# Kernel tuning notes

Measured on AMD Instinct MI355X. Metric: run time of the kernel, lower is better.

The kernel has to match this reference:

```python
import jax, jax.numpy as jnp
import numpy as np

B, T, IN = 8, 1000, 80
CONV = 256
CCEP = 222            # ltv_out_channels
FFT_SIZE = 1024
HOP = 256
WIN = 2 * HOP         # 512
PAD = (FFT_SIZE - CCEP) // 2   # 401
NFFT = 2048


def _conv1d_same(x, W, b, groups):
    # x: (B,T,C); W: (O, C//groups, 3); equivalent to torch Conv1d pad=2 then [1:-1]
    y = jax.lax.conv_general_dilated(
        jnp.transpose(x, (0, 2, 1)), W, (1,), [(1, 1)],
        feature_group_count=groups,
        dimension_numbers=('NCH', 'OIH', 'NCH'))
    return jnp.transpose(y, (0, 2, 1)) + b


def _forward(x, z, W1, b1, W2, b2, W3, b3, W4, b4):
    Bx, Tx, _ = x.shape
    # ---- ConvLayers ----
    h = jax.nn.relu(_conv1d_same(x, W1, b1, 1))
    h = jax.nn.relu(_conv1d_same(h, W2, b2, 8))
    h = jax.nn.relu(_conv1d_same(h, W3, b3, 8))
    ccep = _conv1d_same(h, W4, b4, 1)            # (B,T,222)
    q = jnp.arange(1, CCEP // 2 + 1, dtype=x.dtype)
    quef = jnp.concatenate([q[::-1], q])          # [111..1,1..111]
    ccep = ccep / quef
    # ---- ccep -> impulse (log-magnitude cepstrum -> minimum-ish phase impulse) ----
    c = jnp.pad(ccep, ((0, 0), (0, 0), (PAD, PAD)))           # (B,T,1024)
    Y = jnp.fft.fft(c, n=FFT_SIZE, axis=-1)
    mag = jnp.power(10.0, Y.real)
    imp = jnp.fft.ifft(mag * jnp.exp(1j * Y.imag), n=FFT_SIZE, axis=-1).real  # (B,T,1024)
    # ---- time-varying impulse convolution (cross-correlation per frame) ----
    L = z.shape[-1]
    zz = z.reshape(Bx, 1, L)
    zp = jnp.pad(zz, ((0, 0), (0, 0), (WIN // 2 - 1, WIN // 2)))
    starts = jnp.arange(Tx) * HOP
    frames = zp[:, :, starts[:, None] + jnp.arange(WIN)]       # (B,1,T,512)
    fp = jnp.pad(frames, ((0, 0), (0, 0), (0, 0), (FFT_SIZE // 2 - 1, FFT_SIZE // 2)))  # len 1535
    # corr[s] = sum_k fp[s+k] * imp[k], s in [0,512); linear corr via zero-padded FFT
    Fz = jnp.fft.rfft(fp, n=NFFT, axis=-1)                     # (B,1,T,NFFT//2+1)
    Fy = jnp.fft.rfft(imp, n=NFFT, axis=-1)[:, None]           # (B,1,T,NFFT//2+1)
    corr = jnp.fft.irfft(Fz * jnp.conj(Fy), n=NFFT, axis=-1)[..., :WIN]  # (B,1,T,512)
    # ---- overlap-add ----
    n = jnp.arange(WIN, dtype=x.dtype)
    win = 0.5 * (1.0 - jnp.cos(2.0 * jnp.pi * n / WIN))        # periodic hann, win_norm=1
    zw = corr * win
    l, r = zw[..., :HOP], zw[..., HOP:]
    out = l + jnp.roll(r, 1, axis=2)
    return out.reshape(Bx, 1, Tx * HOP)


def setup_inputs() -> dict:
    key = jax.random.key(0)
    ks = jax.random.split(key, 12)
    x = jax.random.normal(ks[0], (B, T, IN), dtype=jnp.float32)
    z = jax.random.normal(ks[1], (B, 1, T * HOP), dtype=jnp.float32)
    def w(k, o, i, kk, scale):
        return jax.random.normal(k, (o, i, kk), dtype=jnp.float32) * (scale / np.sqrt(i * kk))
    W1 = w(ks[2], CONV, IN, 3, 1.0)
    b1 = jnp.zeros((CONV,), jnp.float32)
    W2 = w(ks[3], CONV, CONV // 8, 3, 1.0)
    b2 = jnp.zeros((CONV,), jnp.float32)
    W3 = w(ks[4], CONV, CONV // 8, 3, 1.0)
    b3 = jnp.zeros((CONV,), jnp.float32)
    W4 = w(ks[5], CCEP, CONV, 3, 0.01)   # small scale keeps 10**(.) well-conditioned
    b4 = jnp.zeros((CCEP,), jnp.float32)
    return {"x": x, "z": z, "W1": W1, "b1": b1, "W2": W2, "b2": b2,
            "W3": W3, "b3": b3, "W4": W4, "b4": b4}


def reference(x, z, W1, b1, W2, b2, W3, b3, W4, b4):
    return _forward(x, z, W1, b1, W2, b2, W3, b3, W4, b4)
```

## Files before the change

### kernel.cpp

```cpp
#include <hip/hip_runtime.h>
#include <hip/hip_bf16.h>

#define T_LEN 1000
#define B_N 8
#define IN_CH 80
#define CONV_CH 256
#define CCEP_N 222

typedef short s8v __attribute__((ext_vector_type(8)));
typedef float f16v __attribute__((ext_vector_type(16)));

#define TWO_PI 6.28318530717958647692f

__global__ __launch_bounds__(256) void k_prep(
    const float* __restrict__ W1, const float* __restrict__ W2,
    const float* __restrict__ W3, const float* __restrict__ W4,
    float* __restrict__ Wt1, float* __restrict__ Wt2, float* __restrict__ Wt3,
    __hip_bfloat16* __restrict__ Wc, float2* __restrict__ twTab,
    float* __restrict__ winTab) {
  const int bid = blockIdx.x, tid = threadIdx.x;
  if (bid < 240) {
    int e = bid * 256 + tid;
    int p = e & 3;
    int r = e >> 2;
    int o = r & 255;
    int s = r >> 8;
    int k = s % 3, i4 = s / 3;
    Wt1[e] = W1[o * 240 + (4 * i4 + p) * 3 + k];
  } else if (bid < 336) {
    int e = (bid - 240) * 256 + tid;
    int p = e & 3;
    int r = e >> 2;
    int o = r & 255;
    int s = r >> 8;
    int k = s % 3, i4 = s / 3;
    Wt2[e] = W2[o * 96 + (4 * i4 + p) * 3 + k];
  } else if (bid < 432) {
    int e = (bid - 336) * 256 + tid;
    int p = e & 3;
    int r = e >> 2;
    int o = r & 255;
    int s = r >> 8;
    int k = s % 3, i4 = s / 3;
    Wt3[e] = W3[o * 96 + (4 * i4 + p) * 3 + k];
  } else if (bid < 1200) {
    int e = (bid - 432) * 256 + tid;
    int kloc = e & 31, n = (e >> 5) & 255, chg = e >> 13;
    int kp = chg * 32 + kloc;
    int kappa = kp >> 8, i = kp & 255;
    float v = 0.f;
    if (n < CCEP_N) {
      float invq = 1.f / (float)((n < 111) ? (111 - n) : (n - 110));
      v = W4[n * 768 + i * 3 + kappa] * invq;
    }
    Wc[e] = __float2bfloat16(v);
  } else {
    int e = (bid - 1200) * 256 + tid;
    if (e < 1020) {
      int Q, off;
      if (e < 768)       { Q = 256; off = 0; }
      else if (e < 960)  { Q = 64;  off = 768; }
      else if (e < 1008) { Q = 16;  off = 960; }
      else               { Q = 4;   off = 1008; }
      int rem = e - off;
      int r = rem / Q, pos = rem - r * Q;
      float ang = (TWO_PI * (float)((r + 1) * pos)) / (float)(4 * Q);
      float s, c;
      sincosf(ang, &s, &c);
      twTab[e] = make_float2(c, s);
    } else if (e < 1532) {
      int n = e - 1020;
      winTab[n] = (0.5f - 0.5f * cosf(TWO_PI * (float)n / 512.f)) * (1.f / 1024.f);
    }
  }
}

template <int NJ, int NI4, int PITCH, int NA2>
__device__ __forceinline__ void conv_acc(const float* __restrict__ abase,
    const float4* __restrict__ wq, float* __restrict__ acc) {
  float4 c0 = wq[0], c1 = wq[256], c2 = wq[512];
  for (int ig = 0; ig < NI4; ++ig) {
    const int nx = (ig + 1 < NI4) ? (ig + 1) : (NI4 - 1);
    float4 n0 = wq[(nx * 3 + 0) * 256];
    float4 n1 = wq[(nx * 3 + 1) * 256];
    float4 n2 = wq[(nx * 3 + 2) * 256];
#pragma unroll
    for (int s = 0; s < 4; ++s) {
      const float* row = abase + (4 * ig + s) * PITCH;
      float a[2 * NA2];
#pragma unroll
      for (int u = 0; u < NA2; ++u)
        *(float2*)&a[2 * u] = *(const float2*)(row + 2 * u);
      const float f0 = ((const float*)&c0)[s];
      const float f1 = ((const float*)&c1)[s];
      const float f2 = ((const float*)&c2)[s];
#pragma unroll
      for (int jl = 0; jl < NJ; ++jl) {
        acc[jl] = fmaf(a[jl], f0, acc[jl]);
        acc[jl] = fmaf(a[jl + 1], f1, acc[jl]);
        acc[jl] = fmaf(a[jl + 2], f2, acc[jl]);
      }
    }
    c0 = n0; c1 = n1; c2 = n2;
  }
}

__global__ __launch_bounds__(256) void k_convall(const float* __restrict__ x,
    const float* __restrict__ Wt1, const float* __restrict__ b1,
    const float* __restrict__ Wt2, const float* __restrict__ b2,
    const float* __restrict__ Wt3, const float* __restrict__ b3,
    __hip_bfloat16* __restrict__ out) {
  const int b = blockIdx.y;
  const int t0 = blockIdx.x * 10;
  const int o = threadIdx.x;
  const int cb = (o >> 5) << 5;
  __shared__ float xs[IN_CH * 18];
  __shared__ float hs1[CONV_CH * 14];
  __shared__ float hs2[CONV_CH * 14];
  for (int e = threadIdx.x; e < 16 * IN_CH; e += 256) {
    int r = e / IN_CH, c = e - r * IN_CH;
    int t = t0 - 3 + r;
    xs[c * 18 + r] = (t >= 0 && t < T_LEN) ? x[(b * T_LEN + t) * IN_CH + c] : 0.f;
  }
  __syncthreads();
  {
    float acc[14];
    const float bv = b1[o];
#pragma unroll
    for (int j = 0; j < 14; j++) acc[j] = bv;
    conv_acc<14, 20, 18, 8>(&xs[0], (const float4*)Wt1 + o, acc);
#pragma unroll
    for (int j = 0; j < 14; j++) {
      int t = t0 - 2 + j;
      hs1[o * 14 + j] = (t >= 0 && t < T_LEN) ? fmaxf(acc[j], 0.f) : 0.f;
    }
  }
  __syncthreads();
  {
    float acc[12];
    const float bv = b2[o];
#pragma unroll
    for (int j = 0; j < 12; j++) acc[j] = bv;
    conv_acc<12, 8, 14, 7>(&hs1[cb * 14], (const float4*)Wt2 + o, acc);
#pragma unroll
    for (int j = 0; j < 12; j++) {
      int t = t0 - 1 + j;
      hs2[o * 14 + j] = (t >= 0 && t < T_LEN) ? fmaxf(acc[j], 0.f) : 0.f;
    }
  }
  __syncthreads();
  {
    float acc[10];
    const float bv = b3[o];
#pragma unroll
    for (int j = 0; j < 10; j++) acc[j] = bv;
    conv_acc<10, 8, 14, 6>(&hs2[cb * 14], (const float4*)Wt3 + o, acc);
#pragma unroll
    for (int j = 0; j < 10; j++)
      out[(b * T_LEN + t0 + j) * CONV_CH + o] = __float2bfloat16(fmaxf(acc[j], 0.f));
  }
}

#define APITCH 264
#define BPITCH 40
#define PSTRIDE 1792000
__global__ __launch_bounds__(256) void k_conv4m(
    const __hip_bfloat16* __restrict__ h3, const __hip_bfloat16* __restrict__ Wc,
    const float* __restrict__ bias, float* __restrict__ Pbase) {
  const int mb = blockIdx.x, b = blockIdx.y, ks = blockIdx.z;
  float* __restrict__ P = Pbase + (size_t)ks * PSTRIDE;
  const int t0 = mb * 64;
  const int tid = threadIdx.x;
  const int w = tid >> 6, lane = tid & 63;
  const int wm = w >> 1, wn = w & 1;
  const int lm = lane & 31, half = lane >> 5;

  __shared__ short h3s[67 * APITCH];
  __shared__ short Bs[2][256 * BPITCH];

  const ushort* h3u = (const ushort*)h3;
  for (int g = tid; g < 67 * 64; g += 256) {
    int rr = g >> 6, c4 = g & 63;
    int t = t0 + rr - 1;
    uint2 v = make_uint2(0u, 0u);
    if (t >= 0 && t < T_LEN)
      v = *(const uint2*)(h3u + (b * T_LEN + t) * CONV_CH + c4 * 4);
    *(uint2*)(h3s + rr * APITCH + c4 * 4) = v;
  }

  const ushort* Wu = (const ushort*)(Wc) + (size_t)(ks * 6) * 8192;
#pragma unroll
  for (int it = 0; it < 4; ++it) {
    int idx = (it * 256 + tid) * 8;
    uint4 v = *(const uint4*)(Wu + idx);
    int n = idx >> 5, kloc = idx & 31;
    *(uint4*)(Bs[0] + n * BPITCH + kloc) = v;
  }
  __syncthreads();

  f16v acc0 = {}, acc1 = {}, acc2 = {}, acc3 = {};

  for (int ch = 0; ch < 6; ++ch) {
    const int p = ch & 1;
    if (ch < 5) {
      const ushort* src = Wu + (ch + 1) * 8192;
#pragma unroll
      for (int it = 0; it < 4; ++it) {
        int idx = (it * 256 + tid) * 8;
        uint4 v = *(const uint4*)(src + idx);
        int n = idx >> 5, kloc = idx & 31;
        *(uint4*)(Bs[p ^ 1] + n * BPITCH + kloc) = v;
      }
    }
#pragma unroll
    for (int s = 0; s < 2; ++s) {
      int k0 = ks * 192 + ch * 32 + s * 16;
      int kappa = k0 >> 8, i0 = k0 & 255;
      s8v a = *(const s8v*)(h3s + (wm * 32 + lm + kappa) * APITCH + i0 + half * 8);
      const short* bp = Bs[p] + (wn * 128 + lm) * BPITCH + s * 16 + half * 8;
      s8v b0 = *(const s8v*)(bp);
      s8v b1 = *(const s8v*)(bp + 32 * BPITCH);
      s8v b2 = *(const s8v*)(bp + 64 * BPITCH);
      s8v b3 = *(const s8v*)(bp + 96 * BPITCH);
      acc0 = __builtin_amdgcn_mfma_f32_32x32x16_bf16(a, b0, acc0, 0, 0, 0);
      acc1 = __builtin_amdgcn_mfma_f32_32x32x16_bf16(a, b1, acc1, 0, 0, 0);
      acc2 = __builtin_amdgcn_mfma_f32_32x32x16_bf16(a, b2, acc2, 0, 0, 0);
      acc3 = __builtin_amdgcn_mfma_f32_32x32x16_bf16(a, b3, acc3, 0, 0, 0);
    }
    __syncthreads();
  }

  const int col = lm;
#pragma unroll
  for (int nt = 0; nt < 4; ++nt) {
    int c = wn * 128 + nt * 32 + col;
    if (c >= CCEP_N) continue;
    float bq = 0.f;
    if (ks == 0) {
      float invq = 1.f / (float)((c < 111) ? (111 - c) : (c - 110));
      bq = bias[c] * invq;
    }
    const f16v* A = (nt == 0) ? &acc0 : (nt == 1) ? &acc1 : (nt == 2) ? &acc2 : &acc3;
#pragma unroll
    for (int reg = 0; reg < 16; ++reg) {
      int row = (reg & 3) + 8 * (reg >> 2) + 4 * half;
      int t = t0 + wm * 32 + row;
      if (t < T_LEN)
        P[(size_t)(b * T_LEN + t) * 224 + c] = (*A)[reg] + bq;
    }
  }
}

__device__ __forceinline__ float2 cmul(float2 a, float2 b) {
  return make_float2(fmaf(a.x, b.x, -(a.y * b.y)), fmaf(a.x, b.y, a.y * b.x));
}
__device__ __forceinline__ float2 cadd(float2 a, float2 b) { return make_float2(a.x + b.x, a.y + b.y); }
__device__ __forceinline__ float2 csub(float2 a, float2 b) { return make_float2(a.x - b.x, a.y - b.y); }

#define LIDX(i) ((i) + ((i) >> 2))

template <int Q, int OFF>
__device__ __forceinline__ void fwd_stage2(float2* __restrict__ A,
    float2* __restrict__ B, const float2* __restrict__ Tw, int j) {
  const int pos = j & (Q - 1);
  const int base = ((j - pos) << 2) + pos;
  float2 e1 = Tw[OFF + pos], e2 = Tw[OFF + Q + pos], e3 = Tw[OFF + 2 * Q + pos];
  const float2 w1 = make_float2(e1.x, -e1.y);
  const float2 w2 = make_float2(e2.x, -e2.y);
  const float2 w3 = make_float2(e3.x, -e3.y);
#pragma unroll
  for (int arr = 0; arr < 2; ++arr) {
    float2* X = arr ? B : A;
    float2 a = X[LIDX(base)], b = X[LIDX(base + Q)];
    float2 cc = X[LIDX(base + 2 * Q)], d = X[LIDX(base + 3 * Q)];
    float2 t0 = cadd(a, cc), t1 = csub(a, cc), t2 = cadd(b, d), bd = csub(b, d);
    float2 t3 = make_float2(bd.y, -bd.x);
    X[LIDX(base)]         = cadd(t0, t2);
    X[LIDX(base + Q)]     = cmul(cadd(t1, t3), w1);
    X[LIDX(base + 2 * Q)] = cmul(csub(t0, t2), w2);
    X[LIDX(base + 3 * Q)] = cmul(csub(t1, t3), w3);
  }
}

template <int Q, int OFF>
__device__ __forceinline__ void inv_stage_t(float2* __restrict__ X,
    const float2* __restrict__ Tw, int j) {
  const int pos = j & (Q - 1);
  const int base = ((j - pos) << 2) + pos;
  const float2 w1 = Tw[OFF + pos];
  const float2 w2 = Tw[OFF + Q + pos];
  const float2 w3 = Tw[OFF + 2 * Q + pos];
  float2 a = X[LIDX(base)];
  float2 b = cmul(X[LIDX(base + Q)], w1);
  float2 cc = cmul(X[LIDX(base + 2 * Q)], w2);
  float2 d = cmul(X[LIDX(base + 3 * Q)], w3);
  float2 t0 = cadd(a, cc), t1 = csub(a, cc), t2 = cadd(b, d), bd = csub(b, d);
  float2 t3 = make_float2(-bd.y, bd.x);
  X[LIDX(base)]         = cadd(t0, t2);
  X[LIDX(base + Q)]     = cadd(t1, t3);
  X[LIDX(base + 2 * Q)] = csub(t0, t2);
  X[LIDX(base + 3 * Q)] = csub(t1, t3);
}

__device__ __forceinline__ int rev4d(int v) {
  return ((v & 3) << 6) | (((v >> 2) & 3) << 4) | (((v >> 4) & 3) << 2) | ((v >> 6) & 3);
}

__global__ __launch_bounds__(256) void k_fft(const float* __restrict__ Pb,
    const float* __restrict__ z, const float2* __restrict__ twg,
    const float* __restrict__ wing, float* __restrict__ out,
    float* __restrict__ sbl, float* __restrict__ sbr) {
  const int u = blockIdx.x, b = blockIdx.y;
  const int tA = 2 * u, tB = tA + 1;
  const int btA = b * T_LEN + tA, btB = btA + 1;
  const int j = threadIdx.x;
  __shared__ float2 WlA[1280];
  __shared__ float2 WlB[1280];
  __shared__ float2 Tws[1020];
  for (int e = j; e < 1020; e += 256) Tws[e] = twg[e];

  const float* zb = z + b * 256000;
  float f0A = 0.f, fS, f1B = 0.f;
  {
    int zi0 = tA * 256 + j - 255;
    f0A = (zi0 >= 0) ? zb[zi0] : 0.f;
    fS = zb[tA * 256 + j + 1];
    int zi2 = tB * 256 + j + 1;
    f1B = (zi2 < 256000) ? zb[zi2] : 0.f;
  }
  float c1A = 0.f, c2A = 0.f, c1B = 0.f, c2B = 0.f;
  if (j >= 145) {
    int mA = btA * 224 + (j - 145), mB = btB * 224 + (j - 145);
    c1A = (Pb[mA] + Pb[mA + PSTRIDE]) + (Pb[mA + 2 * PSTRIDE] + Pb[mA + 3 * PSTRIDE]);
    c1B = (Pb[mB] + Pb[mB + PSTRIDE]) + (Pb[mB + 2 * PSTRIDE] + Pb[mB + 3 * PSTRIDE]);
  }
  if (j < 111) {
    int mA = btA * 224 + (j + 111), mB = btB * 224 + (j + 111);
    c2A = (Pb[mA] + Pb[mA + PSTRIDE]) + (Pb[mA + 2 * PSTRIDE] + Pb[mA + 3 * PSTRIDE]);
    c2B = (Pb[mB] + Pb[mB + PSTRIDE]) + (Pb[mB + 2 * PSTRIDE] + Pb[mB + 3 * PSTRIDE]);
  }
  __syncthreads();

  {
    float2 e1 = Tws[j], e2 = Tws[256 + j], e3 = Tws[512 + j];
    const float2 w1 = make_float2(e1.x, -e1.y);
    const float2 w2 = make_float2(e2.x, -e2.y);
    const float2 w3 = make_float2(e3.x, -e3.y);
    {
      float2 t0 = make_float2(c2A, f0A);
      float2 t1 = make_float2(-c2A, f0A);
      float2 t2 = make_float2(c1A, fS);
      float2 t3 = make_float2(fS, -c1A);
      WlA[LIDX(j)]       = cadd(t0, t2);
      WlA[LIDX(j + 256)] = cmul(cadd(t1, t3), w1);
      WlA[LIDX(j + 512)] = cmul(csub(t0, t2), w2);
      WlA[LIDX(j + 768)] = cmul(csub(t1, t3), w3);
    }
    {
      float2 t0 = make_float2(c2B, fS);
      float2 t1 = make_float2(-c2B, fS);
      float2 t2 = make_float2(c1B, f1B);
      float2 t3 = make_float2(f1B, -c1B);
      WlB[LIDX(j)]       = cadd(t0, t2);
      WlB[LIDX(j + 256)] = cmul(cadd(t1, t3), w1);
      WlB[LIDX(j + 512)] = cmul(csub(t0, t2), w2);
      WlB[LIDX(j + 768)] = cmul(csub(t1, t3), w3);
    }
  }
  __syncthreads();

  fwd_stage2<64, 768>(WlA, WlB, Tws, j);  __syncthreads();
  fwd_stage2<16, 960>(WlA, WlB, Tws, j);  __syncthreads();
  fwd_stage2<4, 1008>(WlA, WlB, Tws, j);  __syncthreads();

  const int base = 4 * j;
  float2 XA[4], XB[4];
  {
    float2 u0 = WlA[LIDX(base)], u1 = WlA[LIDX(base + 1)];
    float2 u2 = WlA[LIDX(base + 2)], u3 = WlA[LIDX(base + 3)];
    float2 t0 = cadd(u0, u2), t1 = csub(u0, u2), t2 = cadd(u1, u3), bd = csub(u1, u3);
    float2 t3 = make_float2(bd.y, -bd.x);
    XA[0] = cadd(t0, t2); XA[1] = cadd(t1, t3); XA[2] = csub(t0, t2); XA[3] = csub(t1, t3);
  }
  {
    float2 u0 = WlB[LIDX(base)], u1 = WlB[LIDX(base + 1)];
    float2 u2 = WlB[LIDX(base + 2)], u3 = WlB[LIDX(base + 3)];
    float2 t0 = cadd(u0, u2), t1 = csub(u0, u2), t2 = cadd(u1, u3), bd = csub(u1, u3);
    float2 t3 = make_float2(bd.y, -bd.x);
    XB[0] = cadd(t0, t2); XB[1] = cadd(t1, t3); XB[2] = csub(t0, t2); XB[3] = csub(t1, t3);
  }
#pragma unroll
  for (int q = 0; q < 4; ++q) { WlA[LIDX(base + q)] = XA[q]; WlB[LIDX(base + q)] = XB[q]; }
  __syncthreads();

  const int r0 = rev4d(j);
  const bool self0 = (r0 == 0);
  const int jp = self0 ? 0 : rev4d((256 - r0) & 255);
  float2 PA[4], PB[4];
#pragma unroll
  for (int q = 0; q < 4; ++q) { PA[q] = WlA[LIDX(4 * jp + q)]; PB[q] = WlB[LIDX(4 * jp + q)]; }
  float2 Z[4];
#pragma unroll
  for (int q = 0; q < 4; ++q) {
    float2 SA, SB;
    {
      float2 A = XA[q];
      float2 Bc = self0 ? PA[(4 - q) & 3] : PA[3 - q];
      float2 Y = make_float2(0.5f * (A.x + Bc.x), 0.5f * (A.y - Bc.y));
      float2 F = make_float2(0.5f * (A.y + Bc.y), -0.5f * (A.x - Bc.x));
      float mag = __expf(Y.x * 2.30258509299404568402f);
      float sy, cy;
      __sincosf(Y.y, &sy, &cy);
      float gr = mag * cy, gi = mag * sy;
      SA = make_float2(fmaf(F.x, gr, F.y * gi), fmaf(F.x, gi, -(F.y * gr)));
    }
    {
      float2 A = XB[q];
      float2 Bc = self0 ? PB[(4 - q) & 3] : PB[3 - q];
      float2 Y = make_float2(0.5f * (A.x + Bc.x), 0.5f * (A.y - Bc.y));
      float2 F = make_float2(0.5f * (A.y + Bc.y), -0.5f * (A.x - Bc.x));
      float mag = __expf(Y.x * 2.30258509299404568402f);
      float sy, cy;
      __sincosf(Y.y, &sy, &cy);
      float gr = mag * cy, gi = mag * sy;
      SB = make_float2(fmaf(F.x, gr, F.y * gi), fmaf(F.x, gi, -(F.y * gr)));
    }
    Z[q] = make_float2(SA.x - SB.y, SA.y + SB.x);
  }
  __syncthreads();

  {
    float2 t0 = cadd(Z[0], Z[2]), t1 = csub(Z[0], Z[2]), t2 = cadd(Z[1], Z[3]), bd = csub(Z[1], Z[3]);
    float2 t3 = make_float2(-bd.y, bd.x);
    WlA[LIDX(base)]     = cadd(t0, t2);
    WlA[LIDX(base + 1)] = cadd(t1, t3);
    WlA[LIDX(base + 2)] = csub(t0, t2);
    WlA[LIDX(base + 3)] = csub(t1, t3);
  }
  __syncthreads();

  inv_stage_t<4, 1008>(WlA, Tws, j);  __syncthreads();
  inv_stage_t<16, 960>(WlA, Tws, j);  __syncthreads();
  inv_stage_t<64, 768>(WlA, Tws, j);  __syncthreads();

  {
    float2 w1 = Tws[j], w2 = Tws[256 + j], w3 = Tws[512 + j];
    float2 a = WlA[LIDX(j)];
    float2 bb = cmul(WlA[LIDX(j + 256)], w1);
    float2 cc = cmul(WlA[LIDX(j + 512)], w2);
    float2 d = cmul(WlA[LIDX(j + 768)], w3);
    float2 t0 = cadd(a, cc), t1 = csub(a, cc), t2 = cadd(bb, d), bd = csub(bb, d);
    float2 t3 = make_float2(-bd.y, bd.x);
    float2 Cj    = cadd(t0, t2);
    float2 Cj256 = cadd(t1, t3);
    int n1 = 511 - j, n2 = 255 - j;
    float wn1 = wing[n1], wn2 = wing[n2];
    float vA_l = Cj256.x * wn2;
    float vAB  = Cj.x * wn1 + Cj256.y * wn2;
    float vB_r = Cj.y * wn1;
    out[(b * T_LEN + tB) * 256 + n2] = vAB;
    int su = (b * 500 + u) * 256 + n2;
    sbl[su] = vA_l;
    sbr[su] = vB_r;
  }
}

__global__ __launch_bounds__(256) void k_even(const float* __restrict__ sbl,
    const float* __restrict__ sbr, float* __restrict__ out) {
  int idx = blockIdx.x * 256 + threadIdx.x;
  int n = idx & 255;
  int bu = idx >> 8;
  int u = bu % 500, b = bu / 500;
  int up = (u == 0) ? 499 : u - 1;
  out[(b * T_LEN + 2 * u) * 256 + n] = sbl[idx] + sbr[(b * 500 + up) * 256 + n];
}

extern "C" void kernel_launch(void* const* d_in, const int* in_sizes, int n_in,
                              void* d_out, int out_size, void* d_ws, size_t ws_size,
                              hipStream_t stream) {
  const float* x  = (const float*)d_in[0];
  const float* z  = (const float*)d_in[1];
  const float* W1 = (const float*)d_in[2];
  const float* b1 = (const float*)d_in[3];
  const float* W2 = (const float*)d_in[4];
  const float* b2 = (const float*)d_in[5];
  const float* W3 = (const float*)d_in[6];
  const float* b3 = (const float*)d_in[7];
  const float* W4 = (const float*)d_in[8];
  const float* b4 = (const float*)d_in[9];

  float* ws   = (float*)d_ws;
  __hip_bfloat16* h3bf = (__hip_bfloat16*)ws;
  float* Pb   = ws + 1024000;
  float* sbl  = ws + 8192000;
  float* sbr  = ws + 9216000;
  float* Wt1  = ws + 10240000;
  float* Wt2  = ws + 10301440;
  float* Wt3  = ws + 10326016;
  __hip_bfloat16* Wc = (__hip_bfloat16*)(ws + 10350592);
  float2* twTab = (float2*)(ws + 10448896);
  float* winTab = ws + 10450944;
  float* out = (float*)d_out;

  dim3 blk(256);
  k_prep<<<1206, blk, 0, stream>>>(W1, W2, W3, W4, Wt1, Wt2, Wt3, Wc,
                                   twTab, winTab);

  dim3 cgrid10(T_LEN / 10, B_N);
  k_convall<<<cgrid10, blk, 0, stream>>>(x, Wt1, b1, Wt2, b2, Wt3, b3, h3bf);
  dim3 g4(16, B_N, 4);
  k_conv4m<<<g4, blk, 0, stream>>>(h3bf, Wc, b4, Pb);
  dim3 gf(T_LEN / 2, B_N);
  k_fft<<<gf, blk, 0, stream>>>(Pb, z, twTab, winTab, out, sbl, sbr);
  k_even<<<4000, blk, 0, stream>>>(sbl, sbr, out);
}
```

Before: 175.6 us.

## Replace fused fp32 conv layers with three fp16 MFMA implicit-GEMM kernels

Replaces the single fused fp32 FMA kernel for the first three conv layers with three launches of a templated fp16 MFMA implicit-GEMM kernel (32x32x16). Input x and weights W1-W3 are converted to fp16 with padded, MFMA-friendly layouts in the prep kernel. Intermediates h1/h2 go through global scratch buffers instead of staying in shared memory. This aims to move the conv arithmetic onto matrix cores, at the cost of extra launches, extra global traffic for intermediates and reduced precision.

```diff
diff --git a/kernel.cpp b/kernel.cpp
--- a/kernel.cpp
+++ b/kernel.cpp
@@ -8,43 +8,44 @@
 #define CCEP_N 222
 
 typedef short s8v __attribute__((ext_vector_type(8)));
+typedef _Float16 h8v __attribute__((ext_vector_type(8)));
 typedef float f16v __attribute__((ext_vector_type(16)));
 
 #define TWO_PI 6.28318530717958647692f
 
 __global__ __launch_bounds__(256) void k_prep(
+    const float* __restrict__ x,
     const float* __restrict__ W1, const float* __restrict__ W2,
     const float* __restrict__ W3, const float* __restrict__ W4,
-    float* __restrict__ Wt1, float* __restrict__ Wt2, float* __restrict__ Wt3,
+    _Float16* __restrict__ xf, _Float16* __restrict__ W1p,
+    _Float16* __restrict__ W2p, _Float16* __restrict__ W3p,
     __hip_bfloat16* __restrict__ Wc, float2* __restrict__ twTab,
     float* __restrict__ winTab) {
   const int bid = blockIdx.x, tid = threadIdx.x;
-  if (bid < 240) {
+  if (bid < 3000) {
     int e = bid * 256 + tid;
-    int p = e & 3;
-    int r = e >> 2;
-    int o = r & 255;
-    int s = r >> 8;
-    int k = s % 3, i4 = s / 3;
-    Wt1[e] = W1[o * 240 + (4 * i4 + p) * 3 + k];
-  } else if (bid < 336) {
-    int e = (bid - 240) * 256 + tid;
-    int p = e & 3;
-    int r = e >> 2;
-    int o = r & 255;
-    int s = r >> 8;
-    int k = s % 3, i4 = s / 3;
-    Wt2[e] = W2[o * 96 + (4 * i4 + p) * 3 + k];
-  } else if (bid < 432) {
-    int e = (bid - 336) * 256 + tid;
-    int p = e & 3;
-    int r = e >> 2;
-    int o = r & 255;
-    int s = r >> 8;
-    int k = s % 3, i4 = s / 3;
-    Wt3[e] = W3[o * 96 + (4 * i4 + p) * 3 + k];
-  } else if (bid < 1200) {
-    int e = (bid - 432) * 256 + tid;
+    int r = e / 96, c = e - r * 96;
+    xf[e] = (c < IN_CH) ? (_Float16)x[r * IN_CH + c] : (_Float16)0.f;
+  } else if (bid < 3288) {
+    int e = (bid - 3000) * 256 + tid;
+    int kloc = e & 31, n = (e >> 5) & 255, chg = e >> 13;
+    int k = chg * 32 + kloc;
+    int kappa = k / 96, i = k - kappa * 96;
+    W1p[e] = (i < IN_CH) ? (_Float16)W1[n * 240 + i * 3 + kappa] : (_Float16)0.f;
+  } else if (bid < 3384) {
+    int e = (bid - 3288) * 256 + tid;
+    int kloc = e & 31, n = (e >> 5) & 255, chg = e >> 13;
+    int k = chg * 32 + kloc;
+    int kappa = k >> 5, iloc = k & 31;
+    W2p[e] = (_Float16)W2[n * 96 + iloc * 3 + kappa];
+  } else if (bid < 3480) {
+    int e = (bid - 3384) * 256 + tid;
+    int kloc = e & 31, n = (e >> 5) & 255, chg = e >> 13;
+    int k = chg * 32 + kloc;
+    int kappa = k >> 5, iloc = k & 31;
+    W3p[e] = (_Float16)W3[n * 96 + iloc * 3 + kappa];
+  } else if (bid < 4248) {
+    int e = (bid - 3480) * 256 + tid;
     int kloc = e & 31, n = (e >> 5) & 255, chg = e >> 13;
     int kp = chg * 32 + kloc;
     int kappa = kp >> 8, i = kp & 255;
@@ -55,7 +56,7 @@
     }
     Wc[e] = __float2bfloat16(v);
   } else {
-    int e = (bid - 1200) * 256 + tid;
+    int e = (bid - 4248) * 256 + tid;
     if (e < 1020) {
       int Q, off;
       if (e < 768)       { Q = 256; off = 0; }
@@ -75,89 +76,75 @@
   }
 }
 
-template <int NJ, int NI4, int PITCH, int NA2>
-__device__ __forceinline__ void conv_acc(const float* __restrict__ abase,
-    const float4* __restrict__ wq, float* __restrict__ acc) {
-  float4 c0 = wq[0], c1 = wq[256], c2 = wq[512];
-  for (int ig = 0; ig < NI4; ++ig) {
-    const int nx = (ig + 1 < NI4) ? (ig + 1) : (NI4 - 1);
-    float4 n0 = wq[(nx * 3 + 0) * 256];
-    float4 n1 = wq[(nx * 3 + 1) * 256];
-    float4 n2 = wq[(nx * 3 + 2) * 256];
-#pragma unroll
-    for (int s = 0; s < 4; ++s) {
-      const float* row = abase + (4 * ig + s) * PITCH;
-      float a[2 * NA2];
-#pragma unroll
-      for (int u = 0; u < NA2; ++u)
-        *(float2*)&a[2 * u] = *(const float2*)(row + 2 * u);
-      const float f0 = ((const float*)&c0)[s];
-      const float f1 = ((const float*)&c1)[s];
-      const float f2 = ((const float*)&c2)[s];
-#pragma unroll
-      for (int jl = 0; jl < NJ; ++jl) {
-        acc[jl] = fmaf(a[jl], f0, acc[jl]);
-        acc[jl] = fmaf(a[jl + 1], f1, acc[jl]);
-        acc[jl] = fmaf(a[jl + 2], f2, acc[jl]);
+template <int NCHG, bool GROUPED, int ACH, int APH, bool OUTBF>
+__global__ __launch_bounds__(256) void k_cgemm(
+    const _Float16* __restrict__ A, const _Float16* __restrict__ Bp,
+    const float* __restrict__ bias, void* __restrict__ outp) {
+  const int mb = blockIdx.x, b = blockIdx.y, z = blockIdx.z;
+  const int t0 = mb * 32;
+  const int tid = threadIdx.x;
+  const int w = tid >> 6, lane = tid & 63;
+  const int lm = lane & 31, half = lane >> 5;
+
+  __shared__ _Float16 As[34 * APH];
+  __shared__ _Float16 Bs[2][128 * 40];
+
+  constexpr int ACOLS = GROUPED ? 128 : ACH;
+  constexpr int NCH4 = ACOLS / 4;
+  for (int e = tid; e < 34 * NCH4; e += 256) {
+    int rr = e / NCH4, c4 = e - rr * NCH4;
+    int t = t0 - 1 + rr;
+    uint2 v = make_uint2(0u, 0u);
+    if (t >= 0 && t < T_LEN)
+      v = *((const uint2*)(A + (size_t)(b * T_LEN + t) * ACH +
+                           (GROUPED ? z * 128 : 0)) + c4);
+    *(uint2*)(As + rr * APH + c4 * 4) = v;
+  }
+  {
+    const _Float16* src = Bp + z * 4096;
+    for (int e = tid; e < 512; e += 256) {
+      int nl = e >> 2, c4 = e & 3;
+      *(uint4*)(Bs[0] + nl * 40 + c4 * 8) = *(const uint4*)(src + nl * 32 + c4 * 8);
+    }
+  }
+  __syncthreads();
+
+  f16v acc = {};
+#pragma unroll
+  for (int chg = 0; chg < NCHG; ++chg) {
+    const int p = chg & 1;
+    if (chg + 1 < NCHG) {
+      const _Float16* src = Bp + (size_t)(chg + 1) * 8192 + z * 4096;
+      for (int e = tid; e < 512; e += 256) {
+        int nl = e >> 2, c4 = e & 3;
+        *(uint4*)(Bs[p ^ 1] + nl * 40 + c4 * 8) = *(const uint4*)(src + nl * 32 + c4 * 8);
       }
     }
-    c0 = n0; c1 = n1; c2 = n2;
-  }
-}
-
-__global__ __launch_bounds__(256) void k_convall(const float* __restrict__ x,
-    const float* __restrict__ Wt1, const float* __restrict__ b1,
-    const float* __restrict__ Wt2, const float* __restrict__ b2,
-    const float* __restrict__ Wt3, const float* __restrict__ b3,
-    __hip_bfloat16* __restrict__ out) {
-  const int b = blockIdx.y;
-  const int t0 = blockIdx.x * 10;
-  const int o = threadIdx.x;
-  const int cb = (o >> 5) << 5;
-  __shared__ float xs[IN_CH * 18];
-  __shared__ float hs1[CONV_CH * 14];
-  __shared__ float hs2[CONV_CH * 14];
-  for (int e = threadIdx.x; e < 16 * IN_CH; e += 256) {
-    int r = e / IN_CH, c = e - r * IN_CH;
-    int t = t0 - 3 + r;
-    xs[c * 18 + r] = (t >= 0 && t < T_LEN) ? x[(b * T_LEN + t) * IN_CH + c] : 0.f;
-  }
-  __syncthreads();
-  {
-    float acc[14];
-    const float bv = b1[o];
-#pragma unroll
-    for (int j = 0; j < 14; j++) acc[j] = bv;
-    conv_acc<14, 20, 18, 8>(&xs[0], (const float4*)Wt1 + o, acc);
-#pragma unroll
-    for (int j = 0; j < 14; j++) {
-      int t = t0 - 2 + j;
-      hs1[o * 14 + j] = (t >= 0 && t < T_LEN) ? fmaxf(acc[j], 0.f) : 0.f;
-    }
-  }
-  __syncthreads();
-  {
-    float acc[12];
-    const float bv = b2[o];
-#pragma unroll
-    for (int j = 0; j < 12; j++) acc[j] = bv;
-    conv_acc<12, 8, 14, 7>(&hs1[cb * 14], (const float4*)Wt2 + o, acc);
-#pragma unroll
-    for (int j = 0; j < 12; j++) {
-      int t = t0 - 1 + j;
-      hs2[o * 14 + j] = (t >= 0 && t < T_LEN) ? fmaxf(acc[j], 0.f) : 0.f;
-    }
-  }
-  __syncthreads();
-  {
-    float acc[10];
-    const float bv = b3[o];
-#pragma unroll
-    for (int j = 0; j < 10; j++) acc[j] = bv;
-    conv_acc<10, 8, 14, 6>(&hs2[cb * 14], (const float4*)Wt3 + o, acc);
-#pragma unroll
-    for (int j = 0; j < 10; j++)
-      out[(b * T_LEN + t0 + j) * CONV_CH + o] = __float2bfloat16(fmaxf(acc[j], 0.f));
+#pragma unroll
+    for (int s = 0; s < 2; ++s) {
+      const int c16 = chg * 2 + s;
+      int kappa, icol;
+      if constexpr (GROUPED) { kappa = c16 >> 1; icol = w * 32 + (c16 & 1) * 16; }
+      else                   { kappa = c16 / 6; icol = (c16 - (c16 / 6) * 6) * 16; }
+      h8v a  = *(const h8v*)(As + (lm + kappa) * APH + icol + half * 8);
+      h8v bf = *(const h8v*)(Bs[p] + (w * 32 + lm) * 40 + s * 16 + half * 8);
+      acc = __builtin_amdgcn_mfma_f32_32x32x16_f16(a, bf, acc, 0, 0, 0);
+    }
+    __syncthreads();
+  }
+
+  const int c = z * 128 + w * 32 + lm;
+  const float bv = bias[c];
+#pragma unroll
+  for (int reg = 0; reg < 16; ++reg) {
+    int row = (reg & 3) + 8 * (reg >> 2) + 4 * half;
+    int t = t0 + row;
+    if (t < T_LEN) {
+      float v = fmaxf(acc[reg] + bv, 0.f);
+      size_t idx = (size_t)(b * T_LEN + t) * CONV_CH + c;
+      if constexpr (OUTBF) ((__hip_bfloat16*)outp)[idx] = __float2bfloat16(v);
+      else                 ((_Float16*)outp)[idx] = (_Float16)v;
+    }
   }
 }
 
@@ -494,20 +481,25 @@
   float* Pb   = ws + 1024000;
   float* sbl  = ws + 8192000;
   float* sbr  = ws + 9216000;
-  float* Wt1  = ws + 10240000;
-  float* Wt2  = ws + 10301440;
-  float* Wt3  = ws + 10326016;
+  _Float16* W1p = (_Float16*)(ws + 10240000);
+  _Float16* W2p = (_Float16*)(ws + 10301440);
+  _Float16* W3p = (_Float16*)(ws + 10326016);
   __hip_bfloat16* Wc = (__hip_bfloat16*)(ws + 10350592);
   float2* twTab = (float2*)(ws + 10448896);
   float* winTab = ws + 10450944;
+  _Float16* xf16 = (_Float16*)(ws + 10451456);
+  _Float16* h1f = (_Float16*)sbl;
+  _Float16* h2f = (_Float16*)sbr;
   float* out = (float*)d_out;
 
   dim3 blk(256);
-  k_prep<<<1206, blk, 0, stream>>>(W1, W2, W3, W4, Wt1, Wt2, Wt3, Wc,
-                                   twTab, winTab);
-
-  dim3 cgrid10(T_LEN / 10, B_N);
-  k_convall<<<cgrid10, blk, 0, stream>>>(x, Wt1, b1, Wt2, b2, Wt3, b3, h3bf);
+  k_prep<<<4254, blk, 0, stream>>>(x, W1, W2, W3, W4, xf16, W1p, W2p, W3p,
+                                   Wc, twTab, winTab);
+
+  dim3 gc(32, B_N, 2);
+  k_cgemm<9, false, 96, 104, false><<<gc, blk, 0, stream>>>(xf16, W1p, b1, (void*)h1f);
+  k_cgemm<3, true, 256, 136, false><<<gc, blk, 0, stream>>>(h1f, W2p, b2, (void*)h2f);
+  k_cgemm<3, true, 256, 136, true><<<gc, blk, 0, stream>>>(h2f, W3p, b3, (void*)h3bf);
   dim3 g4(16, B_N, 4);
   k_conv4m<<<g4, blk, 0, stream>>>(h3bf, Wc, b4, Pb);
   dim3 gf(T_LEN / 2, B_N);
```

After: 158.0 us. 10.0% less time.
